# Performance work log

Hardware: AMD Instinct MI355X
Metric: run time of the kernel (lower is better)

Reference implementation:

```python
import jax, jax.numpy as jnp
import numpy as np

B, N, C = 4, 4096, 256
H, D, K = 8, 32, 16  # heads, dim_head, knn


def setup_inputs() -> dict:
    key = jax.random.key(0)
    ks = jax.random.split(key, 7)
    s = 1.0 / np.sqrt(C)
    return {
        "x": jax.random.normal(ks[0], (B, N, C), dtype=jnp.float32),
        "Wq": jax.random.normal(ks[1], (C, H * D), dtype=jnp.float32) * s,
        "bq": jnp.zeros((H * D,), dtype=jnp.float32),
        "Wk": jax.random.normal(ks[2], (C, H * D), dtype=jnp.float32) * s,
        "bk": jnp.zeros((H * D,), dtype=jnp.float32),
        "Wv": jax.random.normal(ks[3], (C, H * D), dtype=jnp.float32) * s,
        "bv": jnp.zeros((H * D,), dtype=jnp.float32),
    }


def _knn_indices(x):
    # squared euclidean distances per batch: [B, N, N]
    sq = jnp.sum(x * x, axis=-1)
    d2 = sq[:, :, None] + sq[:, None, :] - 2.0 * jnp.einsum("bnc,bmc->bnm", x, x)
    # exclude self-loops (loop=False)
    eye = jnp.eye(x.shape[1], dtype=bool)
    d2 = jnp.where(eye[None], jnp.inf, d2)
    # k nearest neighbors (smallest distance)
    _, idx = jax.lax.top_k(-d2, K)  # [B, N, K]
    return idx


def reference(x, Wq, bq, Wk, bk, Wv, bv):
    idx = _knn_indices(x)  # [B, N, K] neighbor (source) node ids per target node
    # gather neighbor features: [B, N, K, C]
    xj = jax.vmap(lambda xb, ib: xb[ib])(x, idx)
    q = (x @ Wq + bq).reshape(B, N, H, D)           # target-node queries
    ke = (xj @ Wk + bk).reshape(B, N, K, H, D)      # per-edge keys
    ve = (xj @ Wv + bv).reshape(B, N, K, H, D)      # per-edge values
    scale = 1.0 / np.sqrt(D)
    scores = jnp.einsum("bnhd,bnkhd->bnkh", q, ke) * scale
    alpha = jax.nn.softmax(scores, axis=2)          # softmax over each node's K neighbors
    out = jnp.einsum("bnkh,bnkhd->bnhd", alpha, ve)
    return out.reshape(B, N, H * D)
```

## Files before the change

kernel.cpp:

```cpp
#include <hip/hip_runtime.h>
#include <cstdint>
#include <cstddef>

#define N_ 4096
#define C_ 256

typedef _Float16 h8 __attribute__((ext_vector_type(8)));
typedef _Float16 h4 __attribute__((ext_vector_type(4)));
typedef float f4 __attribute__((ext_vector_type(4)));

__device__ __forceinline__ void gl2lds16(const void* g, void* l) {
  __builtin_amdgcn_global_load_lds((const __attribute__((address_space(1))) void*)g,
                                   (__attribute__((address_space(3))) void*)l, 16, 0, 0);
}

__global__ __launch_bounds__(256) void k_prep(const float* __restrict__ x,
                                              float* __restrict__ sq,
                                              _Float16* __restrict__ xh,
                                              _Float16* __restrict__ xl) {
  int wave = threadIdx.x >> 6, lane = threadIdx.x & 63;
  int row = blockIdx.x * 4 + wave;
  size_t off = (size_t)row * C_ + lane * 4;
  float4 v = *(const float4*)(x + off);
  h4 hi; hi[0] = (_Float16)v.x; hi[1] = (_Float16)v.y;
         hi[2] = (_Float16)v.z; hi[3] = (_Float16)v.w;
  h4 lo; lo[0] = (_Float16)(v.x - (float)hi[0]); lo[1] = (_Float16)(v.y - (float)hi[1]);
         lo[2] = (_Float16)(v.z - (float)hi[2]); lo[3] = (_Float16)(v.w - (float)hi[3]);
  *(h4*)(xh + off) = hi;
  *(h4*)(xl + off) = lo;
  float s = v.x * v.x + v.y * v.y + v.z * v.z + v.w * v.w;
  s += __shfl_xor(s, 32); s += __shfl_xor(s, 16); s += __shfl_xor(s, 8);
  s += __shfl_xor(s, 4);  s += __shfl_xor(s, 2);  s += __shfl_xor(s, 1);
  if (lane == 0) sq[row] = s;
}

__global__ __launch_bounds__(256) void k_wsplit(const float* __restrict__ Wq,
                                                const float* __restrict__ Wk,
                                                const float* __restrict__ Wv,
                                                _Float16* __restrict__ wh,
                                                _Float16* __restrict__ wl) {
  int g = blockIdx.x * 256 + threadIdx.x;
  int m = g >> 16, e = g & 65535;
  int k = e >> 8, j = e & 255;
  const float* W = (m == 0) ? Wq : ((m == 1) ? Wk : Wv);
  float v = W[k * 256 + j];
  _Float16 hi = (_Float16)v;
  _Float16 lo = (_Float16)(v - (float)hi);
  wh[m * 65536 + j * 256 + k] = hi;
  wl[m * 65536 + j * 256 + k] = lo;
}

__global__ __launch_bounds__(256, 2) void k_proj(const _Float16* __restrict__ xh,
                                                 const _Float16* __restrict__ xl,
                                                 const _Float16* __restrict__ wh,
                                                 const _Float16* __restrict__ wl,
                                                 const float* __restrict__ bqp,
                                                 const float* __restrict__ bkp,
                                                 const float* __restrict__ bvp,
                                                 float* __restrict__ qf,
                                                 float* __restrict__ kf,
                                                 float* __restrict__ vf) {
  int tid = threadIdx.x;
  int m  = blockIdx.x / 128;
  int rb = blockIdx.x % 128;
  int wave = tid >> 6, lane = tid & 63, quad = lane >> 4, l16 = lane & 15;
  const float* bb = (m == 0) ? bqp : ((m == 1) ? bkp : bvp);
  float* dst      = (m == 0) ? qf  : ((m == 1) ? kf  : vf);
  int row0 = rb * 128 + wave * 32;

  h8 Ah[2][8], Al[2][8];
#pragma unroll
  for (int rt = 0; rt < 2; rt++)
#pragma unroll
    for (int kc = 0; kc < 8; kc++) {
      size_t off = (size_t)(row0 + rt * 16 + l16) * C_ + kc * 32 + quad * 8;
      Ah[rt][kc] = *(const h8*)(xh + off);
      Al[rt][kc] = *(const h8*)(xl + off);
    }
  const _Float16* whm = wh + (size_t)m * 65536;
  const _Float16* wlm = wl + (size_t)m * 65536;

#pragma unroll 1
  for (int cp = 0; cp < 2; cp++) {
    f4 acc[2][8];
#pragma unroll
    for (int rt = 0; rt < 2; rt++)
#pragma unroll
      for (int ct = 0; ct < 8; ct++) acc[rt][ct] = f4{0.f, 0.f, 0.f, 0.f};
#pragma unroll
    for (int kc = 0; kc < 8; kc++) {
#pragma unroll
      for (int ct = 0; ct < 8; ct++) {
        int col = cp * 128 + ct * 16 + l16;
        h8 bh = *(const h8*)(whm + (size_t)col * 256 + kc * 32 + quad * 8);
        h8 bl = *(const h8*)(wlm + (size_t)col * 256 + kc * 32 + quad * 8);
#pragma unroll
        for (int rt = 0; rt < 2; rt++) {
          acc[rt][ct] = __builtin_amdgcn_mfma_f32_16x16x32_f16(Ah[rt][kc], bh, acc[rt][ct], 0, 0, 0);
          acc[rt][ct] = __builtin_amdgcn_mfma_f32_16x16x32_f16(Ah[rt][kc], bl, acc[rt][ct], 0, 0, 0);
          acc[rt][ct] = __builtin_amdgcn_mfma_f32_16x16x32_f16(Al[rt][kc], bh, acc[rt][ct], 0, 0, 0);
        }
      }
    }
#pragma unroll
    for (int rt = 0; rt < 2; rt++)
#pragma unroll
      for (int ct = 0; ct < 8; ct++) {
        int col = cp * 128 + ct * 16 + l16;
        float bias = bb[col];
#pragma unroll
        for (int i = 0; i < 4; i++) {
          int r = row0 + rt * 16 + quad * 4 + i;
          dst[(size_t)r * C_ + col] = acc[rt][ct][i] + bias;
        }
      }
  }
}

__global__ __launch_bounds__(256, 2) void k_knn(const _Float16* __restrict__ xh,
                                                const _Float16* __restrict__ xl,
                                                const float* __restrict__ sq,
                                                double* __restrict__ pd) {
  __shared__ __align__(16) _Float16 Bh[16 * 528];
  __shared__ __align__(16) _Float16 Bl[16 * 528];
  __shared__ __align__(16) float sc[128 * 36];
  __shared__ float sqS[32];

  int tid = threadIdx.x;
  int wave = tid >> 6, lane = tid & 63, quad = lane >> 4, l16 = lane & 15;
  int bid = blockIdx.x;
  int s4 = bid & 3, tile = (bid >> 2) & 31, b = bid >> 7;
  int bN = b * N_, n0 = tile * 128, src0g = s4 * 1024;

  h8 Ah[2][8], Al[2][8];
  int tb = bN + n0 + wave * 32;
#pragma unroll
  for (int rt = 0; rt < 2; rt++)
#pragma unroll
    for (int kc = 0; kc < 8; kc++) {
      size_t off = (size_t)(tb + rt * 16 + l16) * C_ + kc * 32 + quad * 8;
      Ah[rt][kc] = *(const h8*)(xh + off);
      Al[rt][kc] = *(const h8*)(xl + off);
    }
  float sqT[2][4];
#pragma unroll
  for (int rt = 0; rt < 2; rt++)
#pragma unroll
    for (int i = 0; i < 4; i++)
      sqT[rt][i] = sq[tb + rt * 16 + quad * 4 + i];

  double karr[16];
#pragma unroll
  for (int p = 0; p < 16; p++) karr[p] = 1e300;
  int rowo = tid & 127, half = tid >> 7;

  {
    const _Float16* gh = xh + (size_t)(bN + src0g) * C_ + lane * 8;
    const _Float16* gl = xl + (size_t)(bN + src0g) * C_ + lane * 8;
#pragma unroll
    for (int k = 0; k < 4; k++) {
      int seg = wave * 4 + k;
      gl2lds16(gh + seg * 512, &Bh[seg * 528]);
      gl2lds16(gl + seg * 512, &Bl[seg * 528]);
    }
    if (tid < 32) sqS[tid] = sq[bN + src0g + tid];
  }

  int hb0 = ((l16 >> 1) * 528) + ((l16 & 1) * 256) + quad * 8;
  int hb1 = (((16 + l16) >> 1) * 528) + ((l16 & 1) * 256) + quad * 8;

#pragma unroll 1
  for (int ch = 0; ch < 32; ch++) {
    int src0 = src0g + ch * 32;
    __syncthreads();

    f4 acc[2][2];
#pragma unroll
    for (int rt = 0; rt < 2; rt++)
#pragma unroll
      for (int ct = 0; ct < 2; ct++) acc[rt][ct] = f4{0.f, 0.f, 0.f, 0.f};
#pragma unroll
    for (int kc = 0; kc < 8; kc++) {
      h8 bh0 = *(const h8*)(&Bh[hb0 + kc * 32]);
      h8 bh1 = *(const h8*)(&Bh[hb1 + kc * 32]);
      h8 bl0 = *(const h8*)(&Bl[hb0 + kc * 32]);
      h8 bl1 = *(const h8*)(&Bl[hb1 + kc * 32]);
#pragma unroll
      for (int rt = 0; rt < 2; rt++) {
        acc[rt][0] = __builtin_amdgcn_mfma_f32_16x16x32_f16(Ah[rt][kc], bh0, acc[rt][0], 0, 0, 0);
        acc[rt][0] = __builtin_amdgcn_mfma_f32_16x16x32_f16(Ah[rt][kc], bl0, acc[rt][0], 0, 0, 0);
        acc[rt][0] = __builtin_amdgcn_mfma_f32_16x16x32_f16(Al[rt][kc], bh0, acc[rt][0], 0, 0, 0);
        acc[rt][1] = __builtin_amdgcn_mfma_f32_16x16x32_f16(Ah[rt][kc], bh1, acc[rt][1], 0, 0, 0);
        acc[rt][1] = __builtin_amdgcn_mfma_f32_16x16x32_f16(Ah[rt][kc], bl1, acc[rt][1], 0, 0, 0);
        acc[rt][1] = __builtin_amdgcn_mfma_f32_16x16x32_f16(Al[rt][kc], bh1, acc[rt][1], 0, 0, 0);
      }
    }
    float sqSr[2] = {sqS[l16], sqS[16 + l16]};
#pragma unroll
    for (int rt = 0; rt < 2; rt++)
#pragma unroll
      for (int ct = 0; ct < 2; ct++) {
        int c = ct * 16 + l16;
#pragma unroll
        for (int i = 0; i < 4; i++) {
          int r = wave * 32 + rt * 16 + quad * 4 + i;
          float d2 = sqT[rt][i] + sqSr[ct] - 2.0f * acc[rt][ct][i];
          if (n0 + r == src0 + c) d2 = 1e38f;
          sc[r * 36 + c] = d2;
        }
      }
    __syncthreads();

    if (ch < 31) {
      int srcn = src0 + 32;
      const _Float16* gh = xh + (size_t)(bN + srcn) * C_ + lane * 8;
      const _Float16* gl = xl + (size_t)(bN + srcn) * C_ + lane * 8;
#pragma unroll
      for (int k = 0; k < 4; k++) {
        int seg = wave * 4 + k;
        gl2lds16(gh + seg * 512, &Bh[seg * 528]);
        gl2lds16(gl + seg * 512, &Bl[seg * 528]);
      }
      if (tid < 32) sqS[tid] = sq[bN + srcn + tid];
    }

    float dv[16];
#pragma unroll
    for (int k4 = 0; k4 < 4; k4++)
      *(float4*)&dv[k4 * 4] = *(const float4*)(&sc[rowo * 36 + half * 16 + k4 * 4]);
#pragma unroll
    for (int j = 0; j < 16; j++) {
      double key = (double)dv[j];
      key = __longlong_as_double(__double_as_longlong(key) |
                                 (unsigned)(src0 + half * 16 + j));
      if (key < karr[15]) {
#pragma unroll
        for (int p = 15; p >= 1; p--)
          karr[p] = fmin(fmax(key, karr[p - 1]), karr[p]);
        karr[0] = fmin(karr[0], key);
      }
    }
  }

  __syncthreads();
  double* scd = (double*)sc;
  if (tid >= 128) {
#pragma unroll
    for (int p = 0; p < 16; p++) scd[(tid - 128) * 17 + p] = karr[p];
  }
  __syncthreads();
  if (tid < 128) {
#pragma unroll
    for (int j = 0; j < 16; j++) {
      double key = scd[tid * 17 + j];
      if (key < karr[15]) {
#pragma unroll
        for (int p = 15; p >= 1; p--)
          karr[p] = fmin(fmax(key, karr[p - 1]), karr[p]);
        karr[0] = fmin(karr[0], key);
      }
    }
#pragma unroll
    for (int p = 0; p < 16; p++)
      pd[((size_t)bid * 128 + tid) * 16 + p] = karr[p];
  }
}

__global__ __launch_bounds__(256) void k_kmerge(const double* __restrict__ pd,
                                                int* __restrict__ idxo) {
  int g = blockIdx.x * 256 + threadIdx.x;
  int b = g >> 12, n = g & 4095;
  int tile = n >> 7, r = n & 127;
  size_t base[4]; int p[4]; double hd[4];
#pragma unroll
  for (int s = 0; s < 4; s++) {
    base[s] = (size_t)(((b * 32 + tile) * 4 + s) * 128 + r) * 16;
    p[s] = 0;
    hd[s] = pd[base[s]];
  }
#pragma unroll
  for (int k = 0; k < 16; k++) {
    int bs = 0; double bd = hd[0];
#pragma unroll
    for (int s = 1; s < 4; s++) if (hd[s] < bd) { bd = hd[s]; bs = s; }
    idxo[(size_t)g * 16 + k] = (int)(__double_as_longlong(bd) & 0xFFF);
    p[bs]++;
    hd[bs] = (p[bs] < 16) ? pd[base[bs] + p[bs]] : 1e301;
  }
}

__global__ __launch_bounds__(256) void k_attn(const float* __restrict__ qf,
                                              const float* __restrict__ kf,
                                              const float* __restrict__ vf,
                                              const int* __restrict__ idxv,
                                              float* __restrict__ out) {
  int wave = threadIdx.x >> 6, lane = threadIdx.x & 63;
  int g = blockIdx.x * 4 + wave;
  int bN = (g >> 12) << 12;
  float4 q4 = *(const float4*)(qf + (size_t)g * C_ + lane * 4);
  int my = idxv[(size_t)g * 16 + (lane & 15)];
  const float scale = 0.17677669529663687f;

  float s[16];
  float4 vv[16];
#pragma unroll
  for (int j = 0; j < 16; j++) {
    int nb = __shfl(my, j);
    size_t base = (size_t)(bN + nb) * C_ + lane * 4;
    float4 k4 = *(const float4*)(kf + base);
    vv[j] = *(const float4*)(vf + base);
    float p = k4.x * q4.x + k4.y * q4.y + k4.z * q4.z + k4.w * q4.w;
    p += __shfl_xor(p, 1); p += __shfl_xor(p, 2); p += __shfl_xor(p, 4);
    s[j] = p * scale;
  }
  float mx = s[0];
#pragma unroll
  for (int j = 1; j < 16; j++) mx = fmaxf(mx, s[j]);
  float den = 0.f;
#pragma unroll
  for (int j = 0; j < 16; j++) { s[j] = __expf(s[j] - mx); den += s[j]; }
  float inv = 1.0f / den;
  float4 o; o.x = 0.f; o.y = 0.f; o.z = 0.f; o.w = 0.f;
#pragma unroll
  for (int j = 0; j < 16; j++) {
    float w = s[j] * inv;
    o.x = fmaf(w, vv[j].x, o.x); o.y = fmaf(w, vv[j].y, o.y);
    o.z = fmaf(w, vv[j].z, o.z); o.w = fmaf(w, vv[j].w, o.w);
  }
  *(float4*)(out + (size_t)g * C_ + lane * 4) = o;
}

extern "C" void kernel_launch(void* const* d_in, const int* in_sizes, int n_in,
                              void* d_out, int out_size, void* d_ws, size_t ws_size,
                              hipStream_t stream) {
  const float* x  = (const float*)d_in[0];
  const float* Wq = (const float*)d_in[1];
  const float* bq = (const float*)d_in[2];
  const float* Wk = (const float*)d_in[3];
  const float* bk = (const float*)d_in[4];
  const float* Wv = (const float*)d_in[5];
  const float* bv = (const float*)d_in[6];
  float* out = (float*)d_out;

  char* ws = (char*)d_ws;
  float*     sqp  = (float*)(ws + 0);
  _Float16*  xh   = (_Float16*)(ws + 65536);
  _Float16*  xl   = (_Float16*)(ws + 8454144);
  float*     qf   = (float*)(ws + 16842752);
  float*     kf   = (float*)(ws + 33619968);
  float*     vf   = (float*)(ws + 50397184);
  double*    pd   = (double*)(ws + 67174400);
  int*       idxb = (int*)  (ws + 75563008);
  _Float16*  whf  = (_Float16*)(ws + 76611584);
  _Float16*  wlf  = (_Float16*)(ws + 77004800);

  k_prep  <<<4096, 256, 0, stream>>>(x, sqp, xh, xl);
  k_wsplit<<<768,  256, 0, stream>>>(Wq, Wk, Wv, whf, wlf);
  k_proj  <<<384,  256, 0, stream>>>(xh, xl, whf, wlf, bq, bk, bv, qf, kf, vf);
  k_knn   <<<512,  256, 0, stream>>>(xh, xl, sqp, pd);
  k_kmerge<<<64,   256, 0, stream>>>(pd, idxb);
  k_attn  <<<4096, 256, 0, stream>>>(qf, kf, vf, idxb, out);
}
```

Baseline: 350.1 us.

## Use branchless bitonic merge for kNN top-k and split projection columns across blocks

The kNN top-16 maintenance now sorts each batch of 8 candidate keys with a bitonic network and merges it into the running top-16 through a branchless bitonic merge. The final cross-half merge becomes a single bitonic merge. This replaces the per-key branchy insertion and should remove wave divergence, at the cost of doing a fixed amount of compare-exchange work even when no candidate qualifies. Separately, the projection kernel assigns each column half to its own block, doubling the grid to 768 and raising the occupancy hint to 3. That means the A fragments are loaded twice.

```diff
diff --git a/kernel.cpp b/kernel.cpp
--- a/kernel.cpp
+++ b/kernel.cpp
@@ -12,6 +12,42 @@
 __device__ __forceinline__ void gl2lds16(const void* g, void* l) {
   __builtin_amdgcn_global_load_lds((const __attribute__((address_space(1))) void*)g,
                                    (__attribute__((address_space(3))) void*)l, 16, 0, 0);
+}
+
+__device__ __forceinline__ void ce_asc(double& a, double& b) {
+  double mn = fmin(a, b), mx = fmax(a, b);
+  a = mn; b = mx;
+}
+
+__device__ __forceinline__ void sort8_asc(double* c) {
+#pragma unroll
+  for (int k = 2; k <= 8; k <<= 1)
+#pragma unroll
+    for (int j = k >> 1; j > 0; j >>= 1)
+#pragma unroll
+      for (int i = 0; i < 8; i++) {
+        int l = i ^ j;
+        if (l > i) {
+          bool up = ((i & k) == 0);
+          double a = c[i], b = c[l];
+          double mn = fmin(a, b), mx = fmax(a, b);
+          c[i] = up ? mn : mx;
+          c[l] = up ? mx : mn;
+        }
+      }
+}
+
+__device__ __forceinline__ void merge8_top16(double* karr, const double* c) {
+#pragma unroll
+  for (int i = 0; i < 8; i++)
+    karr[8 + i] = fmin(karr[8 + i], c[7 - i]);
+#pragma unroll
+  for (int j = 8; j > 0; j >>= 1)
+#pragma unroll
+    for (int i = 0; i < 16; i++) {
+      int l = i ^ j;
+      if (l > i) ce_asc(karr[i], karr[l]);
+    }
 }
 
 __global__ __launch_bounds__(256) void k_prep(const float* __restrict__ x,
@@ -50,7 +86,7 @@
   wl[m * 65536 + j * 256 + k] = lo;
 }
 
-__global__ __launch_bounds__(256, 2) void k_proj(const _Float16* __restrict__ xh,
+__global__ __launch_bounds__(256, 3) void k_proj(const _Float16* __restrict__ xh,
                                                  const _Float16* __restrict__ xl,
                                                  const _Float16* __restrict__ wh,
                                                  const _Float16* __restrict__ wl,
@@ -61,8 +97,10 @@
                                                  float* __restrict__ kf,
                                                  float* __restrict__ vf) {
   int tid = threadIdx.x;
-  int m  = blockIdx.x / 128;
-  int rb = blockIdx.x % 128;
+  int bid = blockIdx.x;
+  int m   = bid >> 8;
+  int rb  = (bid >> 1) & 127;
+  int cp  = bid & 1;
   int wave = tid >> 6, lane = tid & 63, quad = lane >> 4, l16 = lane & 15;
   const float* bb = (m == 0) ? bqp : ((m == 1) ? bkp : bvp);
   float* dst      = (m == 0) ? qf  : ((m == 1) ? kf  : vf);
@@ -80,41 +118,38 @@
   const _Float16* whm = wh + (size_t)m * 65536;
   const _Float16* wlm = wl + (size_t)m * 65536;
 
-#pragma unroll 1
-  for (int cp = 0; cp < 2; cp++) {
-    f4 acc[2][8];
-#pragma unroll
-    for (int rt = 0; rt < 2; rt++)
-#pragma unroll
-      for (int ct = 0; ct < 8; ct++) acc[rt][ct] = f4{0.f, 0.f, 0.f, 0.f};
-#pragma unroll
-    for (int kc = 0; kc < 8; kc++) {
-#pragma unroll
-      for (int ct = 0; ct < 8; ct++) {
-        int col = cp * 128 + ct * 16 + l16;
-        h8 bh = *(const h8*)(whm + (size_t)col * 256 + kc * 32 + quad * 8);
-        h8 bl = *(const h8*)(wlm + (size_t)col * 256 + kc * 32 + quad * 8);
-#pragma unroll
-        for (int rt = 0; rt < 2; rt++) {
-          acc[rt][ct] = __builtin_amdgcn_mfma_f32_16x16x32_f16(Ah[rt][kc], bh, acc[rt][ct], 0, 0, 0);
-          acc[rt][ct] = __builtin_amdgcn_mfma_f32_16x16x32_f16(Ah[rt][kc], bl, acc[rt][ct], 0, 0, 0);
-          acc[rt][ct] = __builtin_amdgcn_mfma_f32_16x16x32_f16(Al[rt][kc], bh, acc[rt][ct], 0, 0, 0);
-        }
-      }
-    }
-#pragma unroll
-    for (int rt = 0; rt < 2; rt++)
-#pragma unroll
-      for (int ct = 0; ct < 8; ct++) {
-        int col = cp * 128 + ct * 16 + l16;
-        float bias = bb[col];
-#pragma unroll
-        for (int i = 0; i < 4; i++) {
-          int r = row0 + rt * 16 + quad * 4 + i;
-          dst[(size_t)r * C_ + col] = acc[rt][ct][i] + bias;
-        }
-      }
-  }
+  f4 acc[2][8];
+#pragma unroll
+  for (int rt = 0; rt < 2; rt++)
+#pragma unroll
+    for (int ct = 0; ct < 8; ct++) acc[rt][ct] = f4{0.f, 0.f, 0.f, 0.f};
+#pragma unroll
+  for (int kc = 0; kc < 8; kc++) {
+#pragma unroll
+    for (int ct = 0; ct < 8; ct++) {
+      int col = cp * 128 + ct * 16 + l16;
+      h8 bh = *(const h8*)(whm + (size_t)col * 256 + kc * 32 + quad * 8);
+      h8 bl = *(const h8*)(wlm + (size_t)col * 256 + kc * 32 + quad * 8);
+#pragma unroll
+      for (int rt = 0; rt < 2; rt++) {
+        acc[rt][ct] = __builtin_amdgcn_mfma_f32_16x16x32_f16(Ah[rt][kc], bh, acc[rt][ct], 0, 0, 0);
+        acc[rt][ct] = __builtin_amdgcn_mfma_f32_16x16x32_f16(Ah[rt][kc], bl, acc[rt][ct], 0, 0, 0);
+        acc[rt][ct] = __builtin_amdgcn_mfma_f32_16x16x32_f16(Al[rt][kc], bh, acc[rt][ct], 0, 0, 0);
+      }
+    }
+  }
+#pragma unroll
+  for (int rt = 0; rt < 2; rt++)
+#pragma unroll
+    for (int ct = 0; ct < 8; ct++) {
+      int col = cp * 128 + ct * 16 + l16;
+      float bias = bb[col];
+#pragma unroll
+      for (int i = 0; i < 4; i++) {
+        int r = row0 + rt * 16 + quad * 4 + i;
+        dst[(size_t)r * C_ + col] = acc[rt][ct][i] + bias;
+      }
+    }
 }
 
 __global__ __launch_bounds__(256, 2) void k_knn(const _Float16* __restrict__ xh,
@@ -224,21 +259,21 @@
       if (tid < 32) sqS[tid] = sq[bN + srcn + tid];
     }
 
-    float dv[16];
-#pragma unroll
-    for (int k4 = 0; k4 < 4; k4++)
-      *(float4*)&dv[k4 * 4] = *(const float4*)(&sc[rowo * 36 + half * 16 + k4 * 4]);
-#pragma unroll
-    for (int j = 0; j < 16; j++) {
-      double key = (double)dv[j];
-      key = __longlong_as_double(__double_as_longlong(key) |
-                                 (unsigned)(src0 + half * 16 + j));
-      if (key < karr[15]) {
-#pragma unroll
-        for (int p = 15; p >= 1; p--)
-          karr[p] = fmin(fmax(key, karr[p - 1]), karr[p]);
-        karr[0] = fmin(karr[0], key);
-      }
+#pragma unroll
+    for (int bt = 0; bt < 2; bt++) {
+      float dv[8];
+#pragma unroll
+      for (int k4 = 0; k4 < 2; k4++)
+        *(float4*)&dv[k4 * 4] = *(const float4*)(&sc[rowo * 36 + half * 16 + bt * 8 + k4 * 4]);
+      double c8[8];
+#pragma unroll
+      for (int j = 0; j < 8; j++) {
+        double key = (double)dv[j];
+        c8[j] = __longlong_as_double(__double_as_longlong(key) |
+                                     (unsigned)(src0 + half * 16 + bt * 8 + j));
+      }
+      sort8_asc(c8);
+      merge8_top16(karr, c8);
     }
   }
 
@@ -251,15 +286,15 @@
   __syncthreads();
   if (tid < 128) {
 #pragma unroll
-    for (int j = 0; j < 16; j++) {
-      double key = scd[tid * 17 + j];
-      if (key < karr[15]) {
-#pragma unroll
-        for (int p = 15; p >= 1; p--)
-          karr[p] = fmin(fmax(key, karr[p - 1]), karr[p]);
-        karr[0] = fmin(karr[0], key);
-      }
-    }
+    for (int i = 0; i < 16; i++)
+      karr[i] = fmin(karr[i], scd[tid * 17 + (15 - i)]);
+#pragma unroll
+    for (int j = 8; j > 0; j >>= 1)
+#pragma unroll
+      for (int i = 0; i < 16; i++) {
+        int l = i ^ j;
+        if (l > i) ce_asc(karr[i], karr[l]);
+      }
 #pragma unroll
     for (int p = 0; p < 16; p++)
       pd[((size_t)bid * 128 + tid) * 16 + p] = karr[p];
@@ -356,7 +391,7 @@
 
   k_prep  <<<4096, 256, 0, stream>>>(x, sqp, xh, xl);
   k_wsplit<<<768,  256, 0, stream>>>(Wq, Wk, Wv, whf, wlf);
-  k_proj  <<<384,  256, 0, stream>>>(xh, xl, whf, wlf, bq, bk, bv, qf, kf, vf);
+  k_proj  <<<768,  256, 0, stream>>>(xh, xl, whf, wlf, bq, bk, bv, qf, kf, vf);
   k_knn   <<<512,  256, 0, stream>>>(xh, xl, sqp, pd);
   k_kmerge<<<64,   256, 0, stream>>>(pd, idxb);
   k_attn  <<<4096, 256, 0, stream>>>(qf, kf, vf, idxb, out);
```

Measured after the change: 294.9 us. 1.19x faster.
